# Optimization experiments

Hardware: AMD Instinct MI355X
Metric: run time of the kernel (lower is better)

## Reference

```python
import jax, jax.numpy as jnp
import numpy as np

IMG = 128          # img_size
P = 8              # patch_size
H = 768            # model dim (hidden_size)
E = 1536           # GAU expansion dim (2*H), u/v width
K = 128            # key_size
L = (IMG // P) ** 2   # 256 patches
PD = P * P * 3        # 192 patch dim
T = 1000
NL = 24


def sinusoidal_embeddings(pos, dim, base):
    # pos: (L,) -> (L, dim) = [sin | cos]
    half = dim // 2
    freqs = jnp.exp(jnp.arange(half, dtype=jnp.float32) * (-np.log(base) / (half - 1)))
    ang = pos[:, None].astype(jnp.float32) * freqs[None, :]
    return jnp.concatenate([jnp.sin(ang), jnp.cos(ang)], axis=-1)


def make_rope_2d():
    w = IMG // P
    pos = jnp.arange(w * w)
    emb1 = sinusoidal_embeddings(pos // w, 64, 1000.0)
    emb2 = sinusoidal_embeddings(pos % w, 64, 1000.0)
    return jnp.concatenate([emb1, emb2], axis=-1)[None]  # (1, L, 128)


def apply_rope(x, pe):
    # faithful to source: sin_emb = pe[..., :d/2], cos_emb = pe[..., d/2:]
    d = pe.shape[-1]
    sin = pe[..., : d // 2]
    cos = pe[..., d // 2 :]
    x1 = x[..., : d // 2]
    x2 = x[..., d // 2 : d]
    return jnp.concatenate([x1 * cos - x2 * sin, x2 * cos + x1 * sin], axis=-1)


def rmsnorm(x, w):
    rms = jnp.sqrt(jnp.mean(x * x, axis=-1, keepdims=True))
    return x / (rms + 1e-6) * w


def setup_inputs() -> dict:
    key = jax.random.key(0)
    ks = jax.random.split(key, 9)
    B = 16
    s = 0.02
    return {
        "x": jax.random.normal(ks[0], (B, 3, IMG, IMG), dtype=jnp.float32),
        "t_idx": jax.random.randint(ks[1], (B, 1), 0, T),
        "patch_W": jax.random.normal(ks[2], (PD, H), dtype=jnp.float32) * s,
        "t_emb": jax.random.normal(ks[3], (T, H), dtype=jnp.float32) * s,
        "Wuv": jax.random.normal(ks[4], (NL, H, 2 * E + 2 * K), dtype=jnp.float32) * s,
        "Wout": jax.random.normal(ks[5], (NL, E, H), dtype=jnp.float32) * s,
        "gnorm": jnp.ones((NL, H), dtype=jnp.float32),
        "fnorm_w": jnp.ones((H,), dtype=jnp.float32),
        "unpatch_W": jax.random.normal(ks[6], (H, PD), dtype=jnp.float32) * s,
    }


def reference(x, t_idx, patch_W, t_emb, Wuv, Wout, gnorm, fnorm_w, unpatch_W):
    B = x.shape[0]
    g = IMG // P
    # patchify: (B,3,128,128) -> (B, 256, 192)
    xp = x.reshape(B, 3, g, P, g, P).transpose(0, 2, 4, 3, 5, 1).reshape(B, L, PD)
    h = xp @ patch_W + t_emb[t_idx[:, 0]][:, None, :]   # (B, L, H)
    pe = make_rope_2d()                                  # (1, L, 128)
    scale = K ** (-0.5)

    def block(h, params):
        wuv, wout, gn = params
        xn = rmsnorm(h, gn)
        uvqk = xn @ wuv                                  # (B, L, 2E+2K)
        u = jax.nn.silu(uvqk[..., :E])
        v = jax.nn.silu(uvqk[..., E : 2 * E])
        q = apply_rope(uvqk[..., 2 * E : 2 * E + K], pe)
        k = apply_rope(uvqk[..., 2 * E + K :], pe)
        attn = jax.nn.softmax(jnp.einsum('blk,bmk->blm', q, k) * scale, axis=-1)
        o = u * jnp.einsum('blm,bme->ble', attn, v)      # (B, L, E)
        return h + o @ wout, None

    h, _ = jax.lax.scan(block, h, (Wuv, Wout, gnorm))
    h = rmsnorm(h, fnorm_w) @ unpatch_W                  # (B, L, PD)
    # unpatchify: (B,256,192) -> (B,3,128,128)
    out = h.reshape(B, g, g, P, P, 3).transpose(0, 5, 1, 3, 2, 4).reshape(B, 3, IMG, IMG)
    return out
```

## Files before the change

kernel.cpp:

```cpp
#include <hip/hip_runtime.h>
#include <math.h>

#define IMG   128
#define Hdim  768
#define Edim  1536
#define Ltok  256
#define PDim  192
#define NLAY  24
#define Bsz   16
#define Mrows 4096
#define UVW   3328

typedef __bf16 bf16x8 __attribute__((ext_vector_type(8)));
typedef float  f32x4  __attribute__((ext_vector_type(4)));

__device__ __forceinline__ unsigned short f2b(float f) {
    unsigned int u = __float_as_uint(f);
    unsigned int r = (u + 0x7FFF + ((u >> 16) & 1)) >> 16;
    return (unsigned short)r;
}
__device__ __forceinline__ float b2f(unsigned short s) {
    return __uint_as_float((unsigned int)s << 16);
}
__device__ __forceinline__ unsigned int pk2(float lo, float hi) {
    return (unsigned int)f2b(lo) | ((unsigned int)f2b(hi) << 16);
}
__device__ __forceinline__ float silu(float x) {
    return x / (1.0f + expf(-x));
}
__device__ __forceinline__ void gload16(const void* g, void* l) {
    __builtin_amdgcn_global_load_lds(
        (const __attribute__((address_space(1))) void*)g,
        (__attribute__((address_space(3))) void*)l, 16, 0, 0);
}
__device__ __forceinline__ int xcd_wg() {
    int nwg = gridDim.x;
    int orig = blockIdx.x;
    int q8 = nwg >> 3, r8 = nwg & 7;
    int xcd = orig & 7, loc = orig >> 3;
    return (xcd < r8 ? xcd * (q8 + 1) : r8 * (q8 + 1) + (xcd - r8) * q8) + loc;
}

__global__ void pe_kernel(float* __restrict__ pe) {
    int l = blockIdx.x;
    int j = threadIdx.x;
    const float c = -logf(1000.0f) / 31.0f;
    int   sub = j & 31;
    float f   = expf(c * (float)sub);
    float pos = (j < 64) ? (float)(l >> 4) : (float)(l & 15);
    float ang = pos * f;
    pe[l * 128 + j] = ((j & 32) == 0) ? sinf(ang) : cosf(ang);
}

__global__ void patchify_kernel(const float* __restrict__ x, unsigned short* __restrict__ xp) {
    int bc = blockIdx.x;
    int iy = bc & 127;
    int t  = bc >> 7;
    int c  = t % 3;
    int b  = t / 3;
    int ix = threadIdx.x;
    float v = x[((size_t)(b * 3 + c) * IMG + iy) * IMG + ix];
    int gy = iy >> 3, py = iy & 7, gx = ix >> 3, px = ix & 7;
    xp[(size_t)(b * Ltok + gy * 16 + gx) * PDim + (py * 8 + px) * 3 + c] = f2b(v);
}

__global__ void trans_kernel(const float* __restrict__ src, int ldS, long long sS,
                             unsigned short* __restrict__ dst, int ldD, long long sD) {
    src += (long long)blockIdx.z * sS;
    dst += (long long)blockIdx.z * sD;
    __shared__ float t[32][33];
    int c0 = blockIdx.x * 32, r0 = blockIdx.y * 32;
    int tx = threadIdx.x, ty = threadIdx.y;
#pragma unroll
    for (int i = 0; i < 4; ++i)
        t[ty + 8 * i][tx] = src[(size_t)(r0 + ty + 8 * i) * ldS + c0 + tx];
    __syncthreads();
#pragma unroll
    for (int i = 0; i < 4; ++i)
        dst[(size_t)(c0 + ty + 8 * i) * ldD + r0 + tx] = f2b(t[tx][ty + 8 * i]);
}

template <int ACC>
__launch_bounds__(256)
__global__ void gemm_bf16(const unsigned short* __restrict__ A, int lda,
                          const unsigned short* __restrict__ Bt, int ldb,
                          float* __restrict__ C, int ldc,
                          int Kt, int Nt, int nbx) {
    __shared__ unsigned short lsA[2][4096];
    __shared__ unsigned short lsB[2][4096];
    int wg = xcd_wg();
    int bx = wg % nbx, by = wg / nbx;
    int tid  = threadIdx.x;
    int lane = tid & 63, w = tid >> 6, wr = w >> 1, wc = w & 1;
    int row0 = by * 128, col0 = bx * 128;
    int fr = lane & 15, fk = (lane >> 4) * 8;
    f32x4 acc[4][4] = {};

    int c0 = tid, c1 = tid + 256;
    int ar0 = row0 + (c0 >> 2), ar1 = row0 + (c1 >> 2);
    int bn0 = col0 + (c0 >> 2), bn1 = col0 + (c1 >> 2);
    if (bn0 > Nt - 1) bn0 = Nt - 1;
    if (bn1 > Nt - 1) bn1 = Nt - 1;
    int ka0 = (c0 & 3) * 8, ka1 = (c1 & 3) * 8;

#define STAGE_G(buf, k0)                                                       \
    gload16(A  + (size_t)ar0 * lda + (k0) + ka0, &lsA[buf][c0 * 8]);           \
    gload16(A  + (size_t)ar1 * lda + (k0) + ka1, &lsA[buf][c1 * 8]);           \
    gload16(Bt + (size_t)bn0 * ldb + (k0) + ka0, &lsB[buf][c0 * 8]);           \
    gload16(Bt + (size_t)bn1 * ldb + (k0) + ka1, &lsB[buf][c1 * 8]);

    STAGE_G(0, 0);
    __syncthreads();
    int nt = Kt >> 5, cur = 0;
    for (int t = 0; t < nt; ++t) {
        if (t + 1 < nt) { STAGE_G(cur ^ 1, (t + 1) * 32); }
        bf16x8 af[4], bfr[4];
#pragma unroll
        for (int m = 0; m < 4; ++m)
            af[m] = *(const bf16x8*)(&lsA[cur][(wr * 64 + m * 16 + fr) * 32 + fk]);
#pragma unroll
        for (int n = 0; n < 4; ++n)
            bfr[n] = *(const bf16x8*)(&lsB[cur][(wc * 64 + n * 16 + fr) * 32 + fk]);
#pragma unroll
        for (int m = 0; m < 4; ++m)
#pragma unroll
            for (int n = 0; n < 4; ++n)
                acc[m][n] = __builtin_amdgcn_mfma_f32_16x16x32_bf16(af[m], bfr[n], acc[m][n], 0, 0, 0);
        __syncthreads();
        cur ^= 1;
    }
#undef STAGE_G

    int crow = (lane >> 4) * 4;
#pragma unroll
    for (int m = 0; m < 4; ++m) {
#pragma unroll
        for (int n = 0; n < 4; ++n) {
            int gc = col0 + wc * 64 + n * 16 + fr;
            if (gc >= Nt) continue;
#pragma unroll
            for (int j = 0; j < 4; ++j) {
                size_t idx = (size_t)(row0 + wr * 64 + m * 16 + crow + j) * ldc + gc;
                if (ACC) C[idx] += acc[m][n][j];
                else     C[idx]  = acc[m][n][j];
            }
        }
    }
}

__launch_bounds__(256)
__global__ void gemm_wout(const unsigned short* __restrict__ A,
                          const unsigned short* __restrict__ Bt,
                          float* __restrict__ P) {
    __shared__ unsigned short lsA[2][4096];
    __shared__ unsigned short lsB[2][4096];
    int wg = xcd_wg();
    int sk = wg / 192, rem = wg % 192;
    int bx = rem % 6, by = rem / 6;
    int koff = sk * 768;
    float* C = P + (size_t)sk * Mrows * Hdim;
    int tid  = threadIdx.x;
    int lane = tid & 63, w = tid >> 6, wr = w >> 1, wc = w & 1;
    int row0 = by * 128, col0 = bx * 128;
    int fr = lane & 15, fk = (lane >> 4) * 8;
    f32x4 acc[4][4] = {};

    int c0 = tid, c1 = tid + 256;
    int ar0 = row0 + (c0 >> 2), ar1 = row0 + (c1 >> 2);
    int bn0 = col0 + (c0 >> 2), bn1 = col0 + (c1 >> 2);
    int ka0 = koff + (c0 & 3) * 8, ka1 = koff + (c1 & 3) * 8;

#define STAGE_W(buf, k0)                                                       \
    gload16(A  + (size_t)ar0 * Edim + (k0) + ka0, &lsA[buf][c0 * 8]);          \
    gload16(A  + (size_t)ar1 * Edim + (k0) + ka1, &lsA[buf][c1 * 8]);          \
    gload16(Bt + (size_t)bn0 * Edim + (k0) + ka0, &lsB[buf][c0 * 8]);          \
    gload16(Bt + (size_t)bn1 * Edim + (k0) + ka1, &lsB[buf][c1 * 8]);

    STAGE_W(0, 0);
    __syncthreads();
    int cur = 0;
    for (int t = 0; t < 24; ++t) {
        if (t + 1 < 24) { STAGE_W(cur ^ 1, (t + 1) * 32); }
        bf16x8 af[4], bfr[4];
#pragma unroll
        for (int m = 0; m < 4; ++m)
            af[m] = *(const bf16x8*)(&lsA[cur][(wr * 64 + m * 16 + fr) * 32 + fk]);
#pragma unroll
        for (int n = 0; n < 4; ++n)
            bfr[n] = *(const bf16x8*)(&lsB[cur][(wc * 64 + n * 16 + fr) * 32 + fk]);
#pragma unroll
        for (int m = 0; m < 4; ++m)
#pragma unroll
            for (int n = 0; n < 4; ++n)
                acc[m][n] = __builtin_amdgcn_mfma_f32_16x16x32_bf16(af[m], bfr[n], acc[m][n], 0, 0, 0);
        __syncthreads();
        cur ^= 1;
    }
#undef STAGE_W

    int crow = (lane >> 4) * 4;
#pragma unroll
    for (int m = 0; m < 4; ++m) {
#pragma unroll
        for (int n = 0; n < 4; ++n) {
            int gc = col0 + wc * 64 + n * 16 + fr;
#pragma unroll
            for (int j = 0; j < 4; ++j)
                C[(size_t)(row0 + wr * 64 + m * 16 + crow + j) * Hdim + gc] = acc[m][n][j];
        }
    }
}

__launch_bounds__(256)
__global__ void gemm_uvqk(const unsigned short* __restrict__ A,
                          const unsigned short* __restrict__ Bt,
                          unsigned short* __restrict__ uT,
                          unsigned short* __restrict__ vT,
                          unsigned short* __restrict__ qh,
                          unsigned short* __restrict__ kh,
                          const float* __restrict__ pe) {
    __shared__ char smem[64 * 130 * 4];
    int wg = xcd_wg();
    int bx = wg % 26, by = wg / 26;
    int tid  = threadIdx.x;
    int lane = tid & 63, w = tid >> 6, wr = w >> 1, wc = w & 1;
    int row0 = by * 128, col0 = bx * 128;
    int fr = lane & 15, fk = (lane >> 4) * 8;
    f32x4 acc[4][4] = {};

    int c0 = tid, c1 = tid + 256;
    int ar0 = row0 + (c0 >> 2), ar1 = row0 + (c1 >> 2);
    int bn0 = col0 + (c0 >> 2), bn1 = col0 + (c1 >> 2);
    int ka0 = (c0 & 3) * 8, ka1 = (c1 & 3) * 8;

#define STAGE_U(buf, k0)                                                             \
    gload16(A  + (size_t)ar0 * Hdim + (k0) + ka0, smem + (buf) * 8192 + c0 * 16);    \
    gload16(A  + (size_t)ar1 * Hdim + (k0) + ka1, smem + (buf) * 8192 + c1 * 16);    \
    gload16(Bt + (size_t)bn0 * Hdim + (k0) + ka0, smem + 16384 + (buf) * 8192 + c0 * 16); \
    gload16(Bt + (size_t)bn1 * Hdim + (k0) + ka1, smem + 16384 + (buf) * 8192 + c1 * 16);

    STAGE_U(0, 0);
    __syncthreads();
    int cur = 0;
    for (int t = 0; t < Hdim / 32; ++t) {
        if (t + 1 < Hdim / 32) { STAGE_U(cur ^ 1, (t + 1) * 32); }
        const unsigned short* lA = (const unsigned short*)(smem + cur * 8192);
        const unsigned short* lB = (const unsigned short*)(smem + 16384 + cur * 8192);
        bf16x8 af[4], bfr[4];
#pragma unroll
        for (int m = 0; m < 4; ++m)
            af[m] = *(const bf16x8*)(&lA[(wr * 64 + m * 16 + fr) * 32 + fk]);
#pragma unroll
        for (int n = 0; n < 4; ++n)
            bfr[n] = *(const bf16x8*)(&lB[(wc * 64 + n * 16 + fr) * 32 + fk]);
#pragma unroll
        for (int m = 0; m < 4; ++m)
#pragma unroll
            for (int n = 0; n < 4; ++n)
                acc[m][n] = __builtin_amdgcn_mfma_f32_16x16x32_bf16(af[m], bfr[n], acc[m][n], 0, 0, 0);
        __syncthreads();
        cur ^= 1;
    }
#undef STAGE_U

    int crow = (lane >> 4) * 4;

    if (bx >= 24) {
        bool isq = (bx == 24);
        const float scale = isq ? 0.08838834764831845f : 1.0f;
        unsigned short* dst = isq ? qh : kh;
        float* S = (float*)smem;
#pragma unroll
        for (int pass = 0; pass < 2; ++pass) {
            __syncthreads();
            if (wr == pass) {
#pragma unroll
                for (int m = 0; m < 4; ++m)
#pragma unroll
                    for (int n = 0; n < 4; ++n) {
                        int rl = m * 16 + crow;
                        int cl = wc * 64 + n * 16 + fr;
#pragma unroll
                        for (int j = 0; j < 4; ++j)
                            S[(rl + j) * 130 + cl] = acc[m][n][j];
                    }
            }
            __syncthreads();
            int r_loc  = tid >> 2;
            int r_glob = row0 + pass * 64 + r_loc;
            int l = r_glob & 255;
#pragma unroll
            for (int i = 0; i < 16; ++i) {
                int d = (tid & 3) * 16 + i;
                float x1 = S[r_loc * 130 + d];
                float x2 = S[r_loc * 130 + d + 64];
                float sn = pe[l * 128 + d];
                float cs = pe[l * 128 + 64 + d];
                dst[(size_t)r_glob * 128 + d]      = f2b((x1 * cs - x2 * sn) * scale);
                dst[(size_t)r_glob * 128 + d + 64] = f2b((x2 * cs + x1 * sn) * scale);
            }
        }
        return;
    }

#pragma unroll
    for (int m = 0; m < 4; ++m) {
        int row = row0 + wr * 64 + m * 16 + crow;
#pragma unroll
        for (int n = 0; n < 4; ++n) {
            int gc = col0 + wc * 64 + n * 16 + fr;
            ushort4 pk;
            pk.x = f2b(silu(acc[m][n][0]));
            pk.y = f2b(silu(acc[m][n][1]));
            pk.z = f2b(silu(acc[m][n][2]));
            pk.w = f2b(silu(acc[m][n][3]));
            if (bx < 12) {
                *(ushort4*)(uT + (size_t)gc * Mrows + row) = pk;
            } else {
                int e = gc - Edim;
                int b = row >> 8, l = row & 255;
                *(ushort4*)(vT + ((size_t)b * Edim + e) * Ltok + l) = pk;
            }
        }
    }
}

__launch_bounds__(256)
__global__ void fused_attn(const unsigned short* __restrict__ qh,
                           const unsigned short* __restrict__ kh,
                           const unsigned short* __restrict__ vT,
                           const unsigned short* __restrict__ uT,
                           unsigned short* __restrict__ ob) {
    int ec = blockIdx.x, qt = blockIdx.y, b = blockIdx.z;
    int tid  = threadIdx.x;
    int lane = tid & 63, w = tid >> 6;
    int fr = lane & 15, hi = lane >> 4;
    int qbase = b * 256 + qt * 64 + w * 16;

    bf16x8 qf[4];
#pragma unroll
    for (int ks = 0; ks < 4; ++ks)
        qf[ks] = *(const bf16x8*)(qh + (size_t)(qbase + fr) * 128 + ks * 32 + hi * 8);
    f32x4 sacc[16] = {};
#pragma unroll
    for (int mf = 0; mf < 16; ++mf) {
#pragma unroll
        for (int ks = 0; ks < 4; ++ks) {
            bf16x8 kf = *(const bf16x8*)(kh + (size_t)(b * 256 + mf * 16 + fr) * 128 + ks * 32 + hi * 8);
            sacc[mf] = __builtin_amdgcn_mfma_f32_16x16x32_bf16(kf, qf[ks], sacc[mf], 0, 0, 0);
        }
    }

    float mx = -3.4e38f;
#pragma unroll
    for (int mf = 0; mf < 16; ++mf)
#pragma unroll
        for (int j = 0; j < 4; ++j)
            mx = fmaxf(mx, sacc[mf][j]);
    mx = fmaxf(mx, __shfl_xor(mx, 16, 64));
    mx = fmaxf(mx, __shfl_xor(mx, 32, 64));
    float sum = 0.f;
#pragma unroll
    for (int mf = 0; mf < 16; ++mf)
#pragma unroll
        for (int j = 0; j < 4; ++j) {
            float e = expf(sacc[mf][j] - mx);
            sacc[mf][j] = e;
            sum += e;
        }
    sum += __shfl_xor(sum, 16, 64);
    sum += __shfl_xor(sum, 32, 64);
    float inv = 1.0f / sum;

    unsigned int dw[16][2];
#pragma unroll
    for (int mf = 0; mf < 16; ++mf) {
        dw[mf][0] = pk2(sacc[mf][0] * inv, sacc[mf][1] * inv);
        dw[mf][1] = pk2(sacc[mf][2] * inv, sacc[mf][3] * inv);
    }

    int sA = fr + 32 * (hi & 1);
    int sB = sA + 16;
    bool up = (hi >> 1) != 0;
    unsigned int pa[8][4];
#pragma unroll
    for (int ks = 0; ks < 8; ++ks) {
        unsigned int a00 = __shfl((int)dw[2 * ks][0],     sA, 64);
        unsigned int a01 = __shfl((int)dw[2 * ks + 1][0], sA, 64);
        unsigned int a10 = __shfl((int)dw[2 * ks][1],     sA, 64);
        unsigned int a11 = __shfl((int)dw[2 * ks + 1][1], sA, 64);
        unsigned int b00 = __shfl((int)dw[2 * ks][0],     sB, 64);
        unsigned int b01 = __shfl((int)dw[2 * ks + 1][0], sB, 64);
        unsigned int b10 = __shfl((int)dw[2 * ks][1],     sB, 64);
        unsigned int b11 = __shfl((int)dw[2 * ks + 1][1], sB, 64);
        pa[ks][0] = up ? a01 : a00;
        pa[ks][1] = up ? a11 : a10;
        pa[ks][2] = up ? b01 : b00;
        pa[ks][3] = up ? b11 : b10;
    }

    const unsigned short* vb = vT + (size_t)b * Edim * Ltok;
    int e0 = ec * 192;
#pragma unroll 2
    for (int ef = 0; ef < 12; ++ef) {
        int e = e0 + ef * 16 + fr;
        f32x4 oacc = {};
#pragma unroll
        for (int ks = 0; ks < 8; ++ks) {
            bf16x8 vf = *(const bf16x8*)(vb + (size_t)e * Ltok + ks * 32 + hi * 8);
            oacc = __builtin_amdgcn_mfma_f32_16x16x32_bf16(*(const bf16x8*)&pa[ks], vf, oacc, 0, 0, 0);
        }
        ushort4 uv = *(const ushort4*)(uT + (size_t)e * Mrows + qbase + hi * 4);
        ob[(size_t)(qbase + hi * 4 + 0) * Edim + e] = f2b(oacc[0] * b2f(uv.x));
        ob[(size_t)(qbase + hi * 4 + 1) * Edim + e] = f2b(oacc[1] * b2f(uv.y));
        ob[(size_t)(qbase + hi * 4 + 2) * Edim + e] = f2b(oacc[2] * b2f(uv.z));
        ob[(size_t)(qbase + hi * 4 + 3) * Edim + e] = f2b(oacc[3] * b2f(uv.w));
    }
}

__global__ void bias_kernel(float* __restrict__ h, const float* __restrict__ t_emb,
                            const int* __restrict__ t_idx) {
    int r = blockIdx.x;
    int b = r >> 8;
    const float* e = t_emb + (size_t)t_idx[b] * Hdim;
    float* hr = h + (size_t)r * Hdim;
    for (int i = threadIdx.x; i < Hdim; i += 256) hr[i] += e[i];
}

template <int ADD>
__global__ void rmsnorm_kernel(float* __restrict__ x, const float* __restrict__ p,
                               const float* __restrict__ w, unsigned short* __restrict__ y) {
    int r = blockIdx.x * 4 + (threadIdx.x >> 6);
    int lane = threadIdx.x & 63;
    float* xr = x + (size_t)r * Hdim;
    float4 a = *(const float4*)&xr[lane * 4];
    float4 b = *(const float4*)&xr[lane * 4 + 256];
    float4 c = *(const float4*)&xr[lane * 4 + 512];
    if (ADD) {
        const float* p0 = p + (size_t)r * Hdim;
        const float* p1 = p + (size_t)(Mrows + r) * Hdim;
        float4 a0 = *(const float4*)&p0[lane * 4];
        float4 b0 = *(const float4*)&p0[lane * 4 + 256];
        float4 c0 = *(const float4*)&p0[lane * 4 + 512];
        float4 a1 = *(const float4*)&p1[lane * 4];
        float4 b1 = *(const float4*)&p1[lane * 4 + 256];
        float4 c1 = *(const float4*)&p1[lane * 4 + 512];
        a.x += a0.x + a1.x; a.y += a0.y + a1.y; a.z += a0.z + a1.z; a.w += a0.w + a1.w;
        b.x += b0.x + b1.x; b.y += b0.y + b1.y; b.z += b0.z + b1.z; b.w += b0.w + b1.w;
        c.x += c0.x + c1.x; c.y += c0.y + c1.y; c.z += c0.z + c1.z; c.w += c0.w + c1.w;
        *(float4*)&xr[lane * 4]       = a;
        *(float4*)&xr[lane * 4 + 256] = b;
        *(float4*)&xr[lane * 4 + 512] = c;
    }
    float ss = a.x * a.x + a.y * a.y + a.z * a.z + a.w * a.w
             + b.x * b.x + b.y * b.y + b.z * b.z + b.w * b.w
             + c.x * c.x + c.y * c.y + c.z * c.z + c.w * c.w;
#pragma unroll
    for (int o = 1; o < 64; o <<= 1) ss += __shfl_xor(ss, o, 64);
    float s = 1.0f / (sqrtf(ss / (float)Hdim) + 1e-6f);
    float4 wa = *(const float4*)&w[lane * 4];
    float4 wb = *(const float4*)&w[lane * 4 + 256];
    float4 wc = *(const float4*)&w[lane * 4 + 512];
    unsigned short* yr = y + (size_t)r * Hdim;
    ushort4 o0, o1, o2;
    o0.x = f2b(a.x * s * wa.x); o0.y = f2b(a.y * s * wa.y);
    o0.z = f2b(a.z * s * wa.z); o0.w = f2b(a.w * s * wa.w);
    o1.x = f2b(b.x * s * wb.x); o1.y = f2b(b.y * s * wb.y);
    o1.z = f2b(b.z * s * wb.z); o1.w = f2b(b.w * s * wb.w);
    o2.x = f2b(c.x * s * wc.x); o2.y = f2b(c.y * s * wc.y);
    o2.z = f2b(c.z * s * wc.z); o2.w = f2b(c.w * s * wc.w);
    *(ushort4*)&yr[lane * 4]       = o0;
    *(ushort4*)&yr[lane * 4 + 256] = o1;
    *(ushort4*)&yr[lane * 4 + 512] = o2;
}

__global__ void unpatch_kernel(const float* __restrict__ y, float* __restrict__ out) {
    int bc = blockIdx.x;
    int iy = bc & 127;
    int t  = bc >> 7;
    int c  = t % 3;
    int b  = t / 3;
    int ix = threadIdx.x;
    int gy = iy >> 3, py = iy & 7, gx = ix >> 3, px = ix & 7;
    out[((size_t)(b * 3 + c) * IMG + iy) * IMG + ix] =
        y[(size_t)(b * Ltok + gy * 16 + gx) * PDim + (py * 8 + px) * 3 + c];
}

extern "C" void kernel_launch(void* const* d_in, const int* in_sizes, int n_in,
                              void* d_out, int out_size, void* d_ws, size_t ws_size,
                              hipStream_t stream) {
    const float* x        = (const float*)d_in[0];
    const int*   t_idx    = (const int*)  d_in[1];
    const float* patch_W  = (const float*)d_in[2];
    const float* t_emb    = (const float*)d_in[3];
    const float* Wuv      = (const float*)d_in[4];
    const float* Wout     = (const float*)d_in[5];
    const float* gnorm    = (const float*)d_in[6];
    const float* fnorm    = (const float*)d_in[7];
    const float* unpatchW = (const float*)d_in[8];
    float* out = (float*)d_out;

    char* wsb = (char*)d_ws;
    size_t off = 0;
    auto alloc = [&](size_t bytes) { char* p = wsb + off; off += (bytes + 255) & ~(size_t)255; return p; };
    float* pe   = (float*)alloc(256 * 128 * 4);
    float* h    = (float*)alloc((size_t)Mrows * Hdim * 4);
    float* pbuf = (float*)alloc((size_t)2 * Mrows * Hdim * 4);
    float* y    = (float*)alloc((size_t)Mrows * PDim * 4);
    unsigned short* xp   = (unsigned short*)alloc((size_t)Mrows * PDim * 2);
    unsigned short* xn   = (unsigned short*)alloc((size_t)Mrows * Hdim * 2);
    unsigned short* uT   = (unsigned short*)alloc((size_t)Edim * Mrows * 2);
    unsigned short* vT   = (unsigned short*)alloc((size_t)Bsz * Edim * Ltok * 2);
    unsigned short* qh   = (unsigned short*)alloc((size_t)Mrows * 128 * 2);
    unsigned short* kh   = (unsigned short*)alloc((size_t)Mrows * 128 * 2);
    unsigned short* o_bf = (unsigned short*)alloc((size_t)Mrows * Edim * 2);
    unsigned short* WuvT  = (unsigned short*)alloc((size_t)NLAY * UVW * Hdim * 2);
    unsigned short* WoutT = (unsigned short*)alloc((size_t)NLAY * Hdim * Edim * 2);
    unsigned short* patchWT   = (unsigned short*)alloc((size_t)Hdim * PDim * 2);
    unsigned short* unpatchWT = (unsigned short*)alloc((size_t)PDim * Hdim * 2);
    if (off > ws_size) return;

    pe_kernel<<<256, 128, 0, stream>>>(pe);
    patchify_kernel<<<Bsz * 3 * IMG, IMG, 0, stream>>>(x, xp);

    trans_kernel<<<dim3(Hdim / 32, PDim / 32, 1), dim3(32, 8), 0, stream>>>(
        patch_W, Hdim, 0, patchWT, PDim, 0);
    trans_kernel<<<dim3(PDim / 32, Hdim / 32, 1), dim3(32, 8), 0, stream>>>(
        unpatchW, PDim, 0, unpatchWT, Hdim, 0);
    trans_kernel<<<dim3(UVW / 32, Hdim / 32, NLAY), dim3(32, 8), 0, stream>>>(
        Wuv, UVW, (long long)Hdim * UVW, WuvT, Hdim, (long long)UVW * Hdim);
    trans_kernel<<<dim3(Hdim / 32, Edim / 32, NLAY), dim3(32, 8), 0, stream>>>(
        Wout, Hdim, (long long)Edim * Hdim, WoutT, Edim, (long long)Hdim * Edim);

    gemm_bf16<0><<<(Hdim / 128) * (Mrows / 128), 256, 0, stream>>>(
        xp, PDim, patchWT, PDim, h, Hdim, PDim, Hdim, Hdim / 128);
    bias_kernel<<<Mrows, 256, 0, stream>>>(h, t_emb, t_idx);

    rmsnorm_kernel<0><<<Mrows / 4, 256, 0, stream>>>(h, nullptr, gnorm, xn);
    for (int l = 0; l < NLAY; ++l) {
        gemm_uvqk<<<(UVW / 128) * (Mrows / 128), 256, 0, stream>>>(
            xn, WuvT + (size_t)l * UVW * Hdim, uT, vT, qh, kh, pe);
        fused_attn<<<dim3(8, 4, Bsz), 256, 0, stream>>>(qh, kh, vT, uT, o_bf);
        gemm_wout<<<384, 256, 0, stream>>>(
            o_bf, WoutT + (size_t)l * Hdim * Edim, pbuf);
        const float* nw = (l + 1 < NLAY) ? gnorm + (size_t)(l + 1) * Hdim : fnorm;
        rmsnorm_kernel<1><<<Mrows / 4, 256, 0, stream>>>(h, pbuf, nw, xn);
    }

    gemm_bf16<0><<<2 * (Mrows / 128), 256, 0, stream>>>(
        xn, Hdim, unpatchWT, Hdim, y, PDim, Hdim, PDim, 2);
    unpatch_kernel<<<Bsz * 3 * IMG, IMG, 0, stream>>>(y, out);
}
```

Measured before the change: 3.148 ms.

## Rewrite uvqk GEMM with 256x256 tiles, 8 waves, swizzled LDS and ping-pong pipeline

Replaces the 128x128, 4-wave uvqk GEMM with a 256x256 tile kernel using 8 waves, a 64-wide K step, XOR-swizzled LDS layout and a hand-scheduled double-buffered pipeline with interleaved prefetch, barriers and setprio around MFMA bursts. Larger tiles raise arithmetic intensity and cut global reloads, and the swizzle avoids LDS bank conflicts. The q and k RoPE epilogue now runs together in one tile column. Only 208 workgroups run, which risks underfilling the CUs, and the 128KB LDS use limits occupancy.

```diff
diff --git a/kernel.cpp b/kernel.cpp
--- a/kernel.cpp
+++ b/kernel.cpp
@@ -211,110 +211,185 @@
     }
 }
 
-__launch_bounds__(256)
-__global__ void gemm_uvqk(const unsigned short* __restrict__ A,
-                          const unsigned short* __restrict__ Bt,
-                          unsigned short* __restrict__ uT,
-                          unsigned short* __restrict__ vT,
-                          unsigned short* __restrict__ qh,
-                          unsigned short* __restrict__ kh,
-                          const float* __restrict__ pe) {
-    __shared__ char smem[64 * 130 * 4];
+__global__ __launch_bounds__(512, 2)
+void gemm_uvqk8(const unsigned short* __restrict__ A,
+                const unsigned short* __restrict__ Bt,
+                unsigned short* __restrict__ uT,
+                unsigned short* __restrict__ vT,
+                unsigned short* __restrict__ qh,
+                unsigned short* __restrict__ kh,
+                const float* __restrict__ pe) {
+    __shared__ char smem[131072];
     int wg = xcd_wg();
-    int bx = wg % 26, by = wg / 26;
-    int tid  = threadIdx.x;
-    int lane = tid & 63, w = tid >> 6, wr = w >> 1, wc = w & 1;
-    int row0 = by * 128, col0 = bx * 128;
-    int fr = lane & 15, fk = (lane >> 4) * 8;
-    f32x4 acc[4][4] = {};
-
-    int c0 = tid, c1 = tid + 256;
-    int ar0 = row0 + (c0 >> 2), ar1 = row0 + (c1 >> 2);
-    int bn0 = col0 + (c0 >> 2), bn1 = col0 + (c1 >> 2);
-    int ka0 = (c0 & 3) * 8, ka1 = (c1 & 3) * 8;
-
-#define STAGE_U(buf, k0)                                                             \
-    gload16(A  + (size_t)ar0 * Hdim + (k0) + ka0, smem + (buf) * 8192 + c0 * 16);    \
-    gload16(A  + (size_t)ar1 * Hdim + (k0) + ka1, smem + (buf) * 8192 + c1 * 16);    \
-    gload16(Bt + (size_t)bn0 * Hdim + (k0) + ka0, smem + 16384 + (buf) * 8192 + c0 * 16); \
-    gload16(Bt + (size_t)bn1 * Hdim + (k0) + ka1, smem + 16384 + (buf) * 8192 + c1 * 16);
-
-    STAGE_U(0, 0);
-    __syncthreads();
-    int cur = 0;
-    for (int t = 0; t < Hdim / 32; ++t) {
-        if (t + 1 < Hdim / 32) { STAGE_U(cur ^ 1, (t + 1) * 32); }
-        const unsigned short* lA = (const unsigned short*)(smem + cur * 8192);
-        const unsigned short* lB = (const unsigned short*)(smem + 16384 + cur * 8192);
-        bf16x8 af[4], bfr[4];
-#pragma unroll
-        for (int m = 0; m < 4; ++m)
-            af[m] = *(const bf16x8*)(&lA[(wr * 64 + m * 16 + fr) * 32 + fk]);
-#pragma unroll
-        for (int n = 0; n < 4; ++n)
-            bfr[n] = *(const bf16x8*)(&lB[(wc * 64 + n * 16 + fr) * 32 + fk]);
-#pragma unroll
-        for (int m = 0; m < 4; ++m)
-#pragma unroll
-            for (int n = 0; n < 4; ++n)
-                acc[m][n] = __builtin_amdgcn_mfma_f32_16x16x32_bf16(af[m], bfr[n], acc[m][n], 0, 0, 0);
-        __syncthreads();
-        cur ^= 1;
-    }
-#undef STAGE_U
-
-    int crow = (lane >> 4) * 4;
-
-    if (bx >= 24) {
-        bool isq = (bx == 24);
-        const float scale = isq ? 0.08838834764831845f : 1.0f;
-        unsigned short* dst = isq ? qh : kh;
+    int bx = wg % 13, by = wg / 13;
+    int tid = threadIdx.x, lane = tid & 63, wid = tid >> 6;
+    int wm = wid >> 2, wn = wid & 3;
+    int row0 = by * 256, col0 = bx * 256;
+    int fr = lane & 15, hi = lane >> 4;
+    f32x4 acc[8][4] = {};
+
+    int d0 = tid * 16, d1 = d0 + 8192;
+    int s0 = d0 ^ (((d0 >> 7) & 7) << 4);
+    int s1 = d1 ^ (((d1 >> 7) & 7) << 4);
+    int sr0 = s0 >> 7, sc0 = (s0 & 127) >> 1;
+    int sr1 = s1 >> 7, sc1 = (s1 & 127) >> 1;
+
+#define STG_A(bufo, h, kt) do {                                                            \
+    gload16(A + (size_t)(row0 + (h) * 128 + sr0) * Hdim + (kt) * 64 + sc0,                 \
+            smem + (bufo) + (h) * 16384 + d0);                                             \
+    gload16(A + (size_t)(row0 + (h) * 128 + sr1) * Hdim + (kt) * 64 + sc1,                 \
+            smem + (bufo) + (h) * 16384 + d1); } while (0)
+#define STG_B(bufo, h, kt) do {                                                            \
+    gload16(Bt + (size_t)(col0 + (h) * 128 + sr0) * Hdim + (kt) * 64 + sc0,                \
+            smem + (bufo) + 32768 + (h) * 16384 + d0);                                     \
+    gload16(Bt + (size_t)(col0 + (h) * 128 + sr1) * Hdim + (kt) * 64 + sc1,                \
+            smem + (bufo) + 32768 + (h) * 16384 + d1); } while (0)
+
+    int axor = (fr & 7) << 4;
+    int abase = wm * 16384 + fr * 128;
+    int bbase = 32768 + (wn >> 1) * 16384 + ((wn & 1) * 64 + fr) * 128;
+    int koff0 = (hi * 16) ^ axor;
+    int koff1 = (hi * 16 + 64) ^ axor;
+
+    STG_A(0, 0, 0); STG_A(0, 1, 0); STG_B(0, 0, 0); STG_B(0, 1, 0);
+    STG_A(65536, 0, 1); STG_A(65536, 1, 1);
+    asm volatile("s_waitcnt vmcnt(4)" ::: "memory");
+    __builtin_amdgcn_s_barrier();
+    __builtin_amdgcn_sched_barrier(0);
+
+    bf16x8 af[4][2], bf0[2][2], bf1[2][2];
+    const int NKT = Hdim / 64;
+    for (int kt = 0; kt < NKT; ++kt) {
+        int curo = (kt & 1) << 16, nxto = curo ^ 65536;
+        const char* bufc = smem + curo;
+
+#pragma unroll
+        for (int m = 0; m < 4; ++m) {
+            af[m][0] = *(const bf16x8*)(bufc + abase + m * 2048 + koff0);
+            af[m][1] = *(const bf16x8*)(bufc + abase + m * 2048 + koff1);
+        }
+#pragma unroll
+        for (int n = 0; n < 2; ++n) {
+            bf0[n][0] = *(const bf16x8*)(bufc + bbase + n * 2048 + koff0);
+            bf0[n][1] = *(const bf16x8*)(bufc + bbase + n * 2048 + koff1);
+        }
+        if (kt + 1 < NKT) STG_B(nxto, 0, kt + 1);
+        __builtin_amdgcn_s_setprio(1);
+#pragma unroll
+        for (int m = 0; m < 4; ++m)
+#pragma unroll
+            for (int n = 0; n < 2; ++n) {
+                acc[m][n] = __builtin_amdgcn_mfma_f32_16x16x32_bf16(af[m][0], bf0[n][0], acc[m][n], 0, 0, 0);
+                acc[m][n] = __builtin_amdgcn_mfma_f32_16x16x32_bf16(af[m][1], bf0[n][1], acc[m][n], 0, 0, 0);
+            }
+        __builtin_amdgcn_s_setprio(0);
+        __builtin_amdgcn_s_barrier();
+        __builtin_amdgcn_sched_barrier(0);
+
+#pragma unroll
+        for (int n = 0; n < 2; ++n) {
+            bf1[n][0] = *(const bf16x8*)(bufc + bbase + (n + 2) * 2048 + koff0);
+            bf1[n][1] = *(const bf16x8*)(bufc + bbase + (n + 2) * 2048 + koff1);
+        }
+        if (kt + 1 < NKT) STG_B(nxto, 1, kt + 1);
+        __builtin_amdgcn_s_setprio(1);
+#pragma unroll
+        for (int m = 0; m < 4; ++m)
+#pragma unroll
+            for (int n = 0; n < 2; ++n) {
+                acc[m][n + 2] = __builtin_amdgcn_mfma_f32_16x16x32_bf16(af[m][0], bf1[n][0], acc[m][n + 2], 0, 0, 0);
+                acc[m][n + 2] = __builtin_amdgcn_mfma_f32_16x16x32_bf16(af[m][1], bf1[n][1], acc[m][n + 2], 0, 0, 0);
+            }
+        __builtin_amdgcn_s_setprio(0);
+        __builtin_amdgcn_s_barrier();
+        __builtin_amdgcn_sched_barrier(0);
+
+#pragma unroll
+        for (int m = 0; m < 4; ++m) {
+            af[m][0] = *(const bf16x8*)(bufc + abase + (m + 4) * 2048 + koff0);
+            af[m][1] = *(const bf16x8*)(bufc + abase + (m + 4) * 2048 + koff1);
+        }
+        __builtin_amdgcn_s_setprio(1);
+#pragma unroll
+        for (int m = 0; m < 4; ++m)
+#pragma unroll
+            for (int n = 0; n < 2; ++n) {
+                acc[m + 4][n] = __builtin_amdgcn_mfma_f32_16x16x32_bf16(af[m][0], bf0[n][0], acc[m + 4][n], 0, 0, 0);
+                acc[m + 4][n] = __builtin_amdgcn_mfma_f32_16x16x32_bf16(af[m][1], bf0[n][1], acc[m + 4][n], 0, 0, 0);
+            }
+        __builtin_amdgcn_s_setprio(0);
+        __builtin_amdgcn_s_barrier();
+        __builtin_amdgcn_sched_barrier(0);
+
+        if (kt + 2 < NKT) { STG_A(curo, 0, kt + 2); STG_A(curo, 1, kt + 2); }
+        __builtin_amdgcn_s_setprio(1);
+#pragma unroll
+        for (int m = 0; m < 4; ++m)
+#pragma unroll
+            for (int n = 0; n < 2; ++n) {
+                acc[m + 4][n + 2] = __builtin_amdgcn_mfma_f32_16x16x32_bf16(af[m][0], bf1[n][0], acc[m + 4][n + 2], 0, 0, 0);
+                acc[m + 4][n + 2] = __builtin_amdgcn_mfma_f32_16x16x32_bf16(af[m][1], bf1[n][1], acc[m + 4][n + 2], 0, 0, 0);
+            }
+        __builtin_amdgcn_s_setprio(0);
+        asm volatile("s_waitcnt vmcnt(4)" ::: "memory");
+        __builtin_amdgcn_s_barrier();
+        __builtin_amdgcn_sched_barrier(0);
+    }
+#undef STG_A
+#undef STG_B
+
+    if (bx == 12) {
         float* S = (float*)smem;
-#pragma unroll
-        for (int pass = 0; pass < 2; ++pass) {
+        const float qscale = 0.08838834764831845f;
+#pragma unroll
+        for (int p = 0; p < 4; ++p) {
             __syncthreads();
-            if (wr == pass) {
-#pragma unroll
-                for (int m = 0; m < 4; ++m)
+            if (wm == (p >> 1)) {
+#pragma unroll
+                for (int m = 0; m < 4; ++m) {
+                    int mf = (p & 1) * 4 + m;
+                    int rl = m * 16 + hi * 4;
 #pragma unroll
                     for (int n = 0; n < 4; ++n) {
-                        int rl = m * 16 + crow;
-                        int cl = wc * 64 + n * 16 + fr;
+                        int cl = wn * 64 + n * 16 + fr;
 #pragma unroll
                         for (int j = 0; j < 4; ++j)
-                            S[(rl + j) * 130 + cl] = acc[m][n][j];
+                            S[(rl + j) * 256 + cl] = acc[mf][n][j];
                     }
+                }
             }
             __syncthreads();
-            int r_loc  = tid >> 2;
-            int r_glob = row0 + pass * 64 + r_loc;
-            int l = r_glob & 255;
-#pragma unroll
-            for (int i = 0; i < 16; ++i) {
-                int d = (tid & 3) * 16 + i;
-                float x1 = S[r_loc * 130 + d];
-                float x2 = S[r_loc * 130 + d + 64];
-                float sn = pe[l * 128 + d];
-                float cs = pe[l * 128 + 64 + d];
-                dst[(size_t)r_glob * 128 + d]      = f2b((x1 * cs - x2 * sn) * scale);
-                dst[(size_t)r_glob * 128 + d + 64] = f2b((x2 * cs + x1 * sn) * scale);
+            int r = tid >> 3;
+            int dbase = (tid & 7) * 8;
+            int row_g = row0 + p * 64 + r;
+            int l = row_g & 255;
+#pragma unroll
+            for (int i = 0; i < 8; ++i) {
+                int d = dbase + i;
+                float sn = pe[l * 128 + d], cs = pe[l * 128 + 64 + d];
+                float q1 = S[r * 256 + d],       q2 = S[r * 256 + d + 64];
+                float k1 = S[r * 256 + d + 128], k2 = S[r * 256 + d + 192];
+                qh[(size_t)row_g * 128 + d]      = f2b((q1 * cs - q2 * sn) * qscale);
+                qh[(size_t)row_g * 128 + d + 64] = f2b((q2 * cs + q1 * sn) * qscale);
+                kh[(size_t)row_g * 128 + d]      = f2b(k1 * cs - k2 * sn);
+                kh[(size_t)row_g * 128 + d + 64] = f2b(k2 * cs + k1 * sn);
             }
         }
         return;
     }
 
 #pragma unroll
-    for (int m = 0; m < 4; ++m) {
-        int row = row0 + wr * 64 + m * 16 + crow;
-#pragma unroll
-        for (int n = 0; n < 4; ++n) {
-            int gc = col0 + wc * 64 + n * 16 + fr;
+    for (int mf = 0; mf < 8; ++mf) {
+        int row = row0 + wm * 128 + mf * 16 + hi * 4;
+#pragma unroll
+        for (int nf = 0; nf < 4; ++nf) {
+            int gc = col0 + wn * 64 + nf * 16 + fr;
             ushort4 pk;
-            pk.x = f2b(silu(acc[m][n][0]));
-            pk.y = f2b(silu(acc[m][n][1]));
-            pk.z = f2b(silu(acc[m][n][2]));
-            pk.w = f2b(silu(acc[m][n][3]));
-            if (bx < 12) {
+            pk.x = f2b(silu(acc[mf][nf][0]));
+            pk.y = f2b(silu(acc[mf][nf][1]));
+            pk.z = f2b(silu(acc[mf][nf][2]));
+            pk.w = f2b(silu(acc[mf][nf][3]));
+            if (bx < 6) {
                 *(ushort4*)(uT + (size_t)gc * Mrows + row) = pk;
             } else {
                 int e = gc - Edim;
@@ -538,7 +613,7 @@
 
     rmsnorm_kernel<0><<<Mrows / 4, 256, 0, stream>>>(h, nullptr, gnorm, xn);
     for (int l = 0; l < NLAY; ++l) {
-        gemm_uvqk<<<(UVW / 128) * (Mrows / 128), 256, 0, stream>>>(
+        gemm_uvqk8<<<13 * (Mrows / 256), 512, 0, stream>>>(
             xn, WuvT + (size_t)l * UVW * Hdim, uT, vT, qh, kh, pe);
         fused_attn<<<dim3(8, 4, Bsz), 256, 0, stream>>>(qh, kh, vT, uT, o_bf);
         gemm_wout<<<384, 256, 0, stream>>>(
```

Measured after the change: 2.997 ms. -4.8%, faster.
